# Kernel tuning notes

Hardware: AMD Instinct MI355X
Metric: run time of the kernel (lower is better)

The kernel has to match this reference:

```python
import jax, jax.numpy as jnp
import numpy as np

NUM_HEADS = 16
H_SELF = 10  # hardcoded h in forward: first 10 heads self-attend, rest cross-attend
DIM = 1024
HEAD_DIM = DIM // NUM_HEADS
SCALE = HEAD_DIM ** -0.5


def _qkv(x, Wqkv):
    # x: [B, N, C] -> q, k, v each [B, H, N, hd]
    B, N, C = x.shape
    qkv = (x @ Wqkv).reshape(B, N, 3, NUM_HEADS, C // NUM_HEADS).transpose(2, 0, 3, 1, 4)
    return qkv[0], qkv[1], qkv[2]


def _attn(q, k, v):
    # q,k,v: [B, h, N, d]
    scores = jnp.einsum('bhqd,bhkd->bhqk', q, k) * SCALE
    probs = jax.nn.softmax(scores, axis=-1)  # attn_drop_ratio = 0.0
    return jnp.einsum('bhqk,bhkd->bhqd', probs, v)


def _proj(xa, xb, Wproj, bproj):
    # xa: [B, 10, N, d], xb: [B, 6, N, d] -> [B, N, C]
    B = xa.shape[0]
    N = xa.shape[2]
    x = jnp.concatenate([xa, xb], axis=1).transpose(0, 2, 1, 3).reshape(B, N, DIM)
    return x @ Wproj + bproj  # proj_drop_ratio = 0.0


def setup_inputs() -> dict:
    key = jax.random.key(0)
    k0, k1, k2, k3 = jax.random.split(key, 4)
    B, N, C = 16, 577, DIM
    x1 = jax.random.normal(k0, (B, N, C), dtype=jnp.float32)
    x2 = jax.random.normal(k1, (B, N, C), dtype=jnp.float32)
    # nn.Linear(dim, dim*3, bias=False): store as [C, 3C] so y = x @ W
    Wqkv = jax.random.normal(k2, (C, 3 * C), dtype=jnp.float32) * 0.02
    # nn.Linear(dim, dim) has bias by default
    Wproj = jax.random.normal(k3, (C, C), dtype=jnp.float32) * 0.02
    bproj = jnp.zeros((C,), dtype=jnp.float32)
    return {"x1": x1, "x2": x2, "Wqkv": Wqkv, "Wproj": Wproj, "bproj": bproj}


def reference(x1, x2, Wqkv, Wproj, bproj):
    q1, k1, v1 = _qkv(x1, Wqkv)
    q2, k2, v2 = _qkv(x2, Wqkv)
    h = H_SELF
    x11 = _attn(q1[:, :h], k1[:, :h], v1[:, :h])  # self-attn branch of x1
    x12 = _attn(q1[:, h:], k2[:, h:], v2[:, h:])  # cross: q from x1, kv from x2
    x22 = _attn(q2[:, :h], k2[:, :h], v2[:, :h])  # self-attn branch of x2
    x21 = _attn(q2[:, h:], k1[:, h:], v1[:, h:])  # cross: q from x2, kv from x1
    out1 = _proj(x11, x12, Wproj, bproj)
    out2 = _proj(x22, x21, Wproj, bproj)
    return (out1, out2)
```

## Files before the change

### kernel.cpp

```cpp
#include <hip/hip_runtime.h>
#include <hip/hip_bf16.h>
#include <stdint.h>
#include <math.h>

typedef __attribute__((ext_vector_type(8))) short bf16x8;
typedef __attribute__((ext_vector_type(4))) float f32x4;
typedef __attribute__((ext_vector_type(8))) unsigned short ushort8;
typedef __attribute__((ext_vector_type(4))) unsigned int uint4v;
typedef __attribute__((ext_vector_type(2))) unsigned int uint2v;

#define NTOK   9232
#define MROWS  18464
#define MPAD   18688
#define NPADV  640
#define QSCALE 0.18033688011112042f

__device__ __forceinline__ uint16_t f2b(float f) {
  uint32_t u = __builtin_bit_cast(uint32_t, f);
  u += 0x7fffu + ((u >> 16) & 1u);
  return (uint16_t)(u >> 16);
}

__device__ __forceinline__ uint32_t packbf(float lo, float hi) {
  return (uint32_t)f2b(lo) | ((uint32_t)f2b(hi) << 16);
}

__device__ __forceinline__ f32x4 mfma16(bf16x8 a, bf16x8 b, f32x4 c) {
  return __builtin_amdgcn_mfma_f32_16x16x32_bf16(a, b, c, 0, 0, 0);
}

__device__ __forceinline__ void gl_lds16(const void* g, void* l) {
  __builtin_amdgcn_global_load_lds(
      (const __attribute__((address_space(1))) uint32_t*)g,
      (__attribute__((address_space(3))) uint32_t*)l, 16, 0, 0);
}

__global__ void convert_x_kernel(const float* __restrict__ x1,
                                 const float* __restrict__ x2,
                                 uint16_t* __restrict__ Xb) {
  const size_t stride = (size_t)gridDim.x * blockDim.x;
  const size_t total8 = (size_t)MPAD * 1024 / 8;
  for (size_t i = (size_t)blockIdx.x * blockDim.x + threadIdx.x; i < total8; i += stride) {
    const size_t e = i * 8;
    const size_t row = e >> 10;
    ushort8 ov;
    if (row < (size_t)MROWS) {
      const float* src = (row < (size_t)NTOK) ? (x1 + e) : (x2 + (e - (size_t)NTOK * 1024));
      float4 a = *(const float4*)(src);
      float4 b = *(const float4*)(src + 4);
      ov[0] = f2b(a.x); ov[1] = f2b(a.y); ov[2] = f2b(a.z); ov[3] = f2b(a.w);
      ov[4] = f2b(b.x); ov[5] = f2b(b.y); ov[6] = f2b(b.z); ov[7] = f2b(b.w);
    } else {
      ov = (ushort8)0;
    }
    *(ushort8*)(Xb + e) = ov;
  }
}

__global__ void transw_kernel(const float* __restrict__ in, uint16_t* __restrict__ out,
                              int R, int Cc) {
  __shared__ float t[32][33];
  const int r0 = blockIdx.x * 32, c0 = blockIdx.y * 32;
  const int tr = threadIdx.x >> 5, tc = threadIdx.x & 31;
#pragma unroll
  for (int i = 0; i < 4; ++i)
    t[tr + i * 8][tc] = in[(size_t)(r0 + tr + i * 8) * Cc + c0 + tc];
  __syncthreads();
#pragma unroll
  for (int i = 0; i < 4; ++i) {
    const int orow = c0 + tr + i * 8;
    out[(size_t)orow * R + r0 + tc] = f2b(t[tc][tr + i * 8]);
  }
}

__global__ void zero_vpad_kernel(uint16_t* __restrict__ Vtb) {
  const int idx = blockIdx.x * 256 + threadIdx.x;
  for (int i = idx; i < 32768 * 8; i += 256 * 256) {
    const int p = i >> 3;
    const int ch = i & 7;
    *(ushort8*)(Vtb + (size_t)p * NPADV + 576 + ch * 8) = (ushort8)0;
  }
}

#define G256_SETUP                                                             \
  const int srow = tt >> 2;                                        \
  const int schunk = tt & 3;                         \
  const int swc = schunk ^ ((srow >> 1) & 3);                                  \
  const int crs = (c >> 1) & 3;                                                \
  char* aL = (char*)As3;                                                       \
  char* bL = (char*)Bs3;                                                       \
  auto SA = [&](int buf, int t) {                                              \
    _Pragma("unroll")                                                          \
    for (int i = 0; i < 2; ++i) {                                              \
      const int row = i * 128 + srow;                                          \
      gl_lds16(aG + (size_t)row * 2048 + t * 64 + (swc << 4),                  \
               aL + buf * 16384 + row * 64 + (schunk << 4));                   \
    }                                                                          \
  };                                                                           \
  auto SB = [&](int buf, int t) {                                              \
    _Pragma("unroll")                                                          \
    for (int i = 0; i < 2; ++i) {                                              \
      const int row = i * 128 + srow;                                          \
      gl_lds16(bG + (size_t)row * 2048 + t * 64 + (swc << 4),                  \
               bL + buf * 16384 + row * 64 + (schunk << 4));                   \
    }                                                                          \
  };                                                                           \
  auto LDA = [&](int buf, int mi) -> bf16x8 {                                  \
    const int r = wm * 128 + mi * 16 + c;                                      \
    return *(const bf16x8*)(aL + buf * 16384 + r * 64 + ((g ^ crs) << 4));     \
  };                                                                           \
  auto LDB = [&](int buf, int ni) -> bf16x8 {                                  \
    const int r = wn * 64 + ni * 16 + c;                                       \
    return *(const bf16x8*)(bL + buf * 16384 + r * 64 + ((g ^ crs) << 4));     \
  };

#define G256_MFMA_BLOCK(BR)                                                    \
  {                                                                            \
    bf16x8 b0 = LDB(BR, 0), b1 = LDB(BR, 1);                                   \
    bf16x8 b2 = LDB(BR, 2), b3 = LDB(BR, 3);                                   \
    __builtin_amdgcn_s_setprio(1);                                             \
    _Pragma("unroll")                                                          \
    for (int mi = 0; mi < 8; ++mi) {                                           \
      const bf16x8 a0 = LDA(BR, mi);                                           \
      acc[mi][0] = mfma16(a0, b0, acc[mi][0]);                                 \
      acc[mi][1] = mfma16(a0, b1, acc[mi][1]);                                 \
      acc[mi][2] = mfma16(a0, b2, acc[mi][2]);                                 \
      acc[mi][3] = mfma16(a0, b3, acc[mi][3]);                                 \
    }                                                                          \
    __builtin_amdgcn_s_setprio(0);                                             \
  }

#define G256_ITER_S(T, BR, BS)                                                 \
  {                                                                            \
    asm volatile("s_waitcnt vmcnt(4)" ::: "memory");                           \
    __builtin_amdgcn_s_barrier();                                              \
    __builtin_amdgcn_sched_barrier(0);                                         \
    SA(BS, (T) + 2); SB(BS, (T) + 2);                                          \
    G256_MFMA_BLOCK(BR)                                                        \
  }

#define G256_ITER_N(BR, VM)                                                    \
  {                                                                            \
    asm volatile("s_waitcnt vmcnt(" #VM ")" ::: "memory");                     \
    __builtin_amdgcn_s_barrier();                                              \
    __builtin_amdgcn_sched_barrier(0);                                         \
    G256_MFMA_BLOCK(BR)                                                        \
  }

#define G256_KLOOP                                                             \
  G256_SETUP                                                                   \
  SA(0, 0); SB(0, 0); SA(1, 1); SB(1, 1);                                      \
  for (int j = 0; j < 10; ++j) {                                               \
    const int t3 = j * 3;                                                      \
    G256_ITER_S(t3, 0, 2)                                                      \
    G256_ITER_S(t3 + 1, 1, 0)                                                  \
    G256_ITER_S(t3 + 2, 2, 1)                                                  \
  }                                                                            \
  G256_ITER_N(0, 4)                                                            \
  G256_ITER_N(1, 0)

__global__ __launch_bounds__(512, 1) void gemm_qkv_kernel(
    const uint16_t* __restrict__ A, const uint16_t* __restrict__ Bt,
    uint16_t* __restrict__ Qb, uint16_t* __restrict__ Kb, uint16_t* __restrict__ Vtb) {
  __shared__ __align__(128) char smem[98304];
  uint16_t* As3 = (uint16_t*)smem;
  uint16_t* Bs3 = (uint16_t*)(smem + 49152);
  const int tt = threadIdx.x;
  const int w = tt >> 6, l = tt & 63;
  const int c = l & 15, g = l >> 4;
  const int wm = w >> 2, wn = w & 3;
  const int orig = blockIdx.x;
  const int xcd = orig & 7, sub8 = orig >> 3;
  const int work = (xcd < 4 ? xcd * 110 : 440 + (xcd - 4) * 109) + sub8;
  int bm, bn;
  {
    const int stripe = work / 36;
    if (stripe >= 24) { bm = 72; bn = work - 864; }
    else {
      const int r2 = work % 36;
      const int bg = r2 / 12, r3 = r2 % 12;
      bm = stripe * 3 + r3 % 3;
      bn = bg * 4 + r3 / 3;
    }
  }
  f32x4 acc[8][4] = {};
  const char* aG = (const char*)(A + (size_t)bm * 256 * 1024);
  const char* bG = (const char*)(Bt + (size_t)bn * 256 * 1024);

  G256_KLOOP

  const int sArea = bn >> 2;
  __syncthreads();
  if (sArea <= 1) {
    uint16_t* outb = (sArea == 0) ? Qb : Kb;
    const float scale = (sArea == 0) ? QSCALE : 1.0f;
#pragma unroll
    for (int half = 0; half < 2; ++half) {
      if (wm == half) {
        char* wbase = smem + (g * 4) * 544 + (wn * 64 + c) * 2;
#pragma unroll
        for (int mi = 0; mi < 8; ++mi)
#pragma unroll
          for (int r = 0; r < 4; ++r)
#pragma unroll
            for (int ni = 0; ni < 4; ++ni)
              *(uint16_t*)(wbase + mi * 8704 + r * 544 + ni * 32) =
                  f2b(acc[mi][ni][r] * scale);
      }
      __syncthreads();
      {
        const int row = tt >> 2, hp = tt & 3;
        const int R = bm * 256 + half * 128 + row;
        if (R < MROWS) {
          const int src = (R >= NTOK) ? 1 : 0;
          const int rr = R - src * NTOK;
          const int bb = rr / 577;
          const int nn = rr - bb * 577;
          const size_t base0 =
              ((((size_t)src * 16 + bb) * 16 + (bn & 3) * 4) * 577 + nn) * 64;
          const char* rbase = smem + row * 544;
#pragma unroll
          for (int j = 0; j < 8; ++j) {
            const int ch = hp + j * 4;
            const int hh2 = ch >> 3;
            const int dd = (ch & 7) * 8;
            const uint4v v = *(const uint4v*)(rbase + ch * 16);
            *(uint4v*)(outb + base0 + (size_t)hh2 * 577 * 64 + dd) = v;
          }
        }
      }
      __syncthreads();
    }
  } else {
#pragma unroll
    for (int half = 0; half < 2; ++half) {
      if (wm == half) {
        char* wbase = smem + (wn * 64 + c) * 272 + g * 8;
#pragma unroll
        for (int mi = 0; mi < 8; ++mi)
#pragma unroll
          for (int ni = 0; ni < 4; ++ni) {
            const uint2v pw = {packbf(acc[mi][ni][0], acc[mi][ni][1]),
                               packbf(acc[mi][ni][2], acc[mi][ni][3])};
            *(uint2v*)(wbase + ni * 4352 + mi * 32) = pw;
          }
      }
      __syncthreads();
      {
        const int col = tt >> 1, chh = tt & 1;
        const int C = bn * 256 + col;
        const int hh2 = (C >> 6) & 15;
        const int dd = C & 63;
        const char* rbase = smem + col * 272 + chh * 128;
#pragma unroll
        for (int j = 0; j < 8; ++j) {
          const int R0 = bm * 256 + half * 128 + chh * 64 + j * 8;
          if (R0 >= MROWS) continue;
          const int src0 = (R0 >= NTOK) ? 1 : 0;
          const int rr0 = R0 - src0 * NTOK;
          const int bb0 = rr0 / 577;
          const int nn0 = rr0 - bb0 * 577;
          const uint4v v = *(const uint4v*)(rbase + j * 16);
          const uint16_t* pv = (const uint16_t*)&v;
          const bool fast = (R0 + 7 < MROWS) && (nn0 + 8 <= 577) &&
                            (((R0 + 7) >= NTOK ? 1 : 0) == src0);
          if (fast) {
            uint16_t* dst =
                Vtb + ((((size_t)src0 * 16 + bb0) * 16 + hh2) * 64 + dd) * NPADV + nn0;
#pragma unroll
            for (int e = 0; e < 8; ++e) dst[e] = pv[e];
          } else {
#pragma unroll
            for (int e = 0; e < 8; ++e) {
              const int R = R0 + e;
              if (R >= MROWS) break;
              const int s = (R >= NTOK) ? 1 : 0;
              const int rr = R - s * NTOK;
              const int b2 = rr / 577;
              const int n2 = rr - b2 * 577;
              Vtb[((((size_t)s * 16 + b2) * 16 + hh2) * 64 + dd) * NPADV + n2] = pv[e];
            }
          }
        }
      }
      __syncthreads();
    }
  }
}

#define GEMM_TRI_SETUP                                                         \
  const int srow4 = tt >> 2;                                        \
  const int schunk = tt & 3;                         \
  const int swc = schunk ^ ((srow4 >> 1) & 3);                                 \
  const int crs = (c >> 1) & 3;                                                \
  char* aL = (char*)As3;                                                       \
  char* bL = (char*)Bs3;                                                       \
  auto SA = [&](int buf, int t) {                                              \
    _Pragma("unroll")                                                          \
    for (int i = 0; i < 2; ++i) {                                              \
      const int row = i * 64 + srow4;                                          \
      gl_lds16(aG + (size_t)row * 2048 + t * 64 + (swc << 4),                  \
               aL + buf * 8192 + row * 64 + (schunk << 4));                    \
    }                                                                          \
  };                                                                           \
  auto SB = [&](int buf, int t) {                                              \
    _Pragma("unroll")                                                          \
    for (int i = 0; i < 2; ++i) {                                              \
      const int row = i * 64 + srow4;                                          \
      gl_lds16(bG + (size_t)row * 2048 + t * 64 + (swc << 4),                  \
               bL + buf * 8192 + row * 64 + (schunk << 4));                    \
    }                                                                          \
  };                                                                           \
  auto LDA = [&](int buf, int mi) -> bf16x8 {                                  \
    const int r = wm * 64 + mi * 16 + c;                                       \
    return *(const bf16x8*)(aL + buf * 8192 + r * 64 + ((g ^ crs) << 4));      \
  };                                                                           \
  auto LDB = [&](int buf, int ni) -> bf16x8 {                                  \
    const int r = wn * 64 + ni * 16 + c;                                       \
    return *(const bf16x8*)(bL + buf * 8192 + r * 64 + ((g ^ crs) << 4));      \
  };

#define G_MFMA_BLOCK(BR)                                                       \
  {                                                                            \
    bf16x8 b0 = LDB(BR, 0), b1 = LDB(BR, 1);                                   \
    bf16x8 b2 = LDB(BR, 2), b3 = LDB(BR, 3);                                   \
    __builtin_amdgcn_s_setprio(1);                                             \
    _Pragma("unroll")                                                          \
    for (int mi = 0; mi < 4; ++mi) {                                           \
      const bf16x8 a0 = LDA(BR, mi);                                           \
      acc[mi][0] = mfma16(a0, b0, acc[mi][0]);                                 \
      acc[mi][1] = mfma16(a0, b1, acc[mi][1]);                                 \
      acc[mi][2] = mfma16(a0, b2, acc[mi][2]);                                 \
      acc[mi][3] = mfma16(a0, b3, acc[mi][3]);                                 \
    }                                                                          \
    __builtin_amdgcn_s_setprio(0);                                             \
  }

#define G_ITER_S(T, BR, BS)                                                    \
  {                                                                            \
    asm volatile("s_waitcnt vmcnt(4)" ::: "memory");                           \
    __builtin_amdgcn_s_barrier();                                              \
    __builtin_amdgcn_sched_barrier(0);                                         \
    SA(BS, (T) + 2); SB(BS, (T) + 2);                                          \
    G_MFMA_BLOCK(BR)                                                           \
  }

#define G_ITER_N(BR, VM)                                                       \
  {                                                                            \
    asm volatile("s_waitcnt vmcnt(" #VM ")" ::: "memory");                     \
    __builtin_amdgcn_s_barrier();                                              \
    __builtin_amdgcn_sched_barrier(0);                                         \
    G_MFMA_BLOCK(BR)                                                           \
  }

#define GEMM_TRI_KLOOP                                                         \
  GEMM_TRI_SETUP                                                               \
  SA(0, 0); SB(0, 0); SA(1, 1); SB(1, 1);                                      \
  for (int j = 0; j < 10; ++j) {                                               \
    const int t3 = j * 3;                                                      \
    G_ITER_S(t3, 0, 2)                                                         \
    G_ITER_S(t3 + 1, 1, 0)                                                     \
    G_ITER_S(t3 + 2, 2, 1)                                                     \
  }                                                                            \
  G_ITER_N(0, 4)                                                               \
  G_ITER_N(1, 0)

#define KVB 64
#define ATT_NT 10
__global__ __launch_bounds__(256, 2) void attn_kernel(
    const uint16_t* __restrict__ Qb, const uint16_t* __restrict__ Kb,
    const uint16_t* __restrict__ Vtb, uint16_t* __restrict__ O) {
  __shared__ __align__(128) char smem[73728];
  const int tid = threadIdx.x;
  const int w = tid >> 6, l = tid & 63;
  const int c = l & 15, g = l >> 4;
  const int bid = blockIdx.x;
  const int qc = bid & 1;
  const int p = bid >> 1;
  const int h = p & 15, b = (p >> 4) & 15, o = p >> 8;
  const int kvsrc = (h < 10) ? o : (1 - o);
  const uint16_t* qp = Qb + (((size_t)o * 16 + b) * 16 + h) * 577 * 64;
  const uint16_t* kp = Kb + (((size_t)kvsrc * 16 + b) * 16 + h) * 577 * 64;
  const uint16_t* vp = Vtb + (((size_t)kvsrc * 16 + b) * 16 + h) * 64 * NPADV;

  const int qbase = qc * 320 + w * 80;

  const int sub = l >> 3;
  const int colEl = (((l & 7) ^ sub) << 3);
  char* KsA = smem;
  char* VsA = smem + 16384;
  char* Pb  = smem + 32768 + w * 10240;
  const int rs = (c & 7) << 4;

  bf16x8 Qf[5][2];
#pragma unroll
  for (int qt = 0; qt < 5; ++qt) {
    const int qrow = min(qbase + qt * 16 + c, 576);
    const uint16_t* qr = qp + (size_t)qrow * 64 + g * 8;
    Qf[qt][0] = *(const bf16x8*)(qr);
    Qf[qt][1] = *(const bf16x8*)(qr + 32);
  }

  f32x4 acc[4][5] = {};
  float m_run[5] = {-3.0e38f, -3.0e38f, -3.0e38f, -3.0e38f, -3.0e38f};
  float l_run[5] = {0.f, 0.f, 0.f, 0.f, 0.f};

  auto STAGE = [&](int buf, int kv0) {
#pragma unroll
    for (int i = 0; i < 2; ++i) {
      const int j = w * 2 + i;
      const int row = j * 8 + sub;
      const int gk = min(kv0 + row, 576);
      gl_lds16(kp + (size_t)gk * 64 + colEl, KsA + buf * 8192 + j * 1024 + l * 16);
      gl_lds16(vp + (size_t)row * NPADV + kv0 + colEl, VsA + buf * 8192 + j * 1024 + l * 16);
    }
  };

  STAGE(0, 0);
  __syncthreads();

  for (int t = 0; t < ATT_NT; ++t) {
    if (t < ATT_NT - 1) STAGE((t + 1) & 1, (t + 1) * KVB);
    {
      const char* Kt = KsA + (t & 1) * 8192;
      const char* Vt = VsA + (t & 1) * 8192;
      bf16x8 Kf[4][2];
#pragma unroll
      for (int kt = 0; kt < 4; ++kt) {
        const char* kr = Kt + (kt * 16 + c) * 128;
        Kf[kt][0] = *(const bf16x8*)(kr + ((g * 16) ^ rs));
        Kf[kt][1] = *(const bf16x8*)(kr + ((64 + g * 16) ^ rs));
      }
      float alpha_[5];
#pragma unroll
      for (int qt = 0; qt < 5; ++qt) {
        f32x4 s[4];
#pragma unroll
        for (int kt = 0; kt < 4; ++kt) {
          f32x4 z = {0.f, 0.f, 0.f, 0.f};
          z = mfma16(Kf[kt][0], Qf[qt][0], z);
          z = mfma16(Kf[kt][1], Qf[qt][1], z);
          s[kt] = z;
        }
        if (t == ATT_NT - 1) {
#pragma unroll
          for (int kt = 0; kt < 4; ++kt)
#pragma unroll
            for (int r = 0; r < 4; ++r) {
              if (kt == 0 && r == 0) { if (g > 0) s[kt][r] = -3.0e38f; }
              else s[kt][r] = -3.0e38f;
            }
        }
        float mt = s[0][0];
#pragma unroll
        for (int kt = 0; kt < 4; ++kt)
#pragma unroll
          for (int r = 0; r < 4; ++r) mt = fmaxf(mt, s[kt][r]);
        mt = fmaxf(mt, __shfl_xor(mt, 16));
        mt = fmaxf(mt, __shfl_xor(mt, 32));
        const float mnew = fmaxf(m_run[qt], mt);
        const float al = exp2f(m_run[qt] - mnew);
        m_run[qt] = mnew;
        alpha_[qt] = al;
        float lt = 0.f;
#pragma unroll
        for (int kt = 0; kt < 4; ++kt)
#pragma unroll
          for (int r = 0; r < 4; ++r) {
            const float pv = exp2f(s[kt][r] - mnew);
            s[kt][r] = pv;
            lt += pv;
          }
        lt += __shfl_xor(lt, 16);
        lt += __shfl_xor(lt, 32);
        l_run[qt] = l_run[qt] * al + lt;
        const int rowOff = (qt * 16 + c) * 128;
#pragma unroll
        for (int kt = 0; kt < 4; ++kt) {
          const uint2v pw = {packbf(s[kt][0], s[kt][1]), packbf(s[kt][2], s[kt][3])};
          *(uint2v*)(Pb + rowOff + ((kt * 32 + g * 8) ^ rs)) = pw;
        }
      }
#pragma unroll
      for (int dt = 0; dt < 4; ++dt)
#pragma unroll
        for (int qt = 0; qt < 5; ++qt)
#pragma unroll
          for (int r = 0; r < 4; ++r) acc[dt][qt][r] *= alpha_[qt];
      bf16x8 pf[5][2];
#pragma unroll
      for (int qt = 0; qt < 5; ++qt) {
        const char* pr = Pb + (qt * 16 + c) * 128;
        pf[qt][0] = *(const bf16x8*)(pr + ((g * 16) ^ rs));
        pf[qt][1] = *(const bf16x8*)(pr + ((64 + g * 16) ^ rs));
      }
#pragma unroll
      for (int dt = 0; dt < 4; ++dt) {
        const char* vr = Vt + (dt * 16 + c) * 128;
        const bf16x8 v0 = *(const bf16x8*)(vr + ((g * 16) ^ rs));
        const bf16x8 v1 = *(const bf16x8*)(vr + ((64 + g * 16) ^ rs));
#pragma unroll
        for (int qt = 0; qt < 5; ++qt) {
          acc[dt][qt] = mfma16(v0, pf[qt][0], acc[dt][qt]);
          acc[dt][qt] = mfma16(v1, pf[qt][1], acc[dt][qt]);
        }
      }
    }
    __syncthreads();
  }

  {
#pragma unroll
    for (int qt = 0; qt < 5; ++qt) {
      const float inv = 1.0f / l_run[qt];
      const int rowOff = (qt * 16 + c) * 128;
#pragma unroll
      for (int dt = 0; dt < 4; ++dt) {
        const uint2v pw = {packbf(acc[dt][qt][0] * inv, acc[dt][qt][1] * inv),
                           packbf(acc[dt][qt][2] * inv, acc[dt][qt][3] * inv)};
        *(uint2v*)(Pb + rowOff + ((dt * 32 + g * 8) ^ rs)) = pw;
      }
    }
    const size_t obase = ((size_t)o * NTOK + (size_t)b * 577) * 1024 + h * 64;
#pragma unroll
    for (int pass = 0; pass < 10; ++pass) {
      const int row = pass * 8 + (l >> 3);
      const int tok = qbase + row;
      const uint4v vv = *(const uint4v*)(Pb + row * 128 + (((l & 7) * 16) ^ ((row & 7) << 4)));
      if (tok <= 576)
        *(uint4v*)(O + obase + (size_t)tok * 1024 + (l & 7) * 8) = vv;
    }
  }
}

__global__ __launch_bounds__(256, 3) void gemm_proj_kernel(
    const uint16_t* __restrict__ A, const uint16_t* __restrict__ Bt,
    const float* __restrict__ bias, float* __restrict__ out) {
  __shared__ uint16_t As3[3][4096];
  __shared__ uint16_t Bs3[3][4096];
  const int tt = threadIdx.x;
  const int w = tt >> 6, l = tt & 63;
  const int c = l & 15, g = l >> 4;
  const int wgid = blockIdx.x;
  const int work = (wgid & 7) * 145 + (wgid >> 3);
  int bm, bn;
  {
    const int stripe = work / 48;
    if (stripe >= 24) { bm = 144; bn = work - 24 * 48; }
    else { const int r3 = work % 48; bm = stripe * 6 + r3 % 6; bn = r3 / 6; }
  }
  const int wm = w >> 1, wn = w & 1;
  f32x4 acc[4][4] = {};
  const char* aG = (const char*)(A + (size_t)bm * 128 * 1024);
  const char* bG = (const char*)(Bt + (size_t)bn * 128 * 1024);

  GEMM_TRI_KLOOP

#pragma unroll
  for (int mi = 0; mi < 4; ++mi) {
#pragma unroll
    for (int r = 0; r < 4; ++r) {
      const int R = bm * 128 + wm * 64 + mi * 16 + g * 4 + r;
      if (R >= MROWS) continue;
#pragma unroll
      for (int ni = 0; ni < 4; ++ni) {
        const int C = bn * 128 + wn * 64 + ni * 16 + c;
        out[(size_t)R * 1024 + C] = acc[mi][ni][r] + bias[C];
      }
    }
  }
}

extern "C" void kernel_launch(void* const* d_in, const int* in_sizes, int n_in,
                              void* d_out, int out_size, void* d_ws, size_t ws_size,
                              hipStream_t stream) {
  (void)in_sizes; (void)n_in; (void)out_size; (void)ws_size;
  const float* x1    = (const float*)d_in[0];
  const float* x2    = (const float*)d_in[1];
  const float* Wqkv  = (const float*)d_in[2];
  const float* Wproj = (const float*)d_in[3];
  const float* bproj = (const float*)d_in[4];
  float* out = (float*)d_out;

  char* ws = (char*)d_ws;
  size_t off = 0;
  auto alloc = [&](size_t bytes) -> char* {
    char* p = ws + off;
    off += (bytes + 255) & ~(size_t)255;
    return p;
  };
  uint16_t* Xb     = (uint16_t*)alloc((size_t)MPAD * 1024 * 2);
  uint16_t* Wqkvt  = (uint16_t*)alloc((size_t)3072 * 1024 * 2);
  uint16_t* Wprojt = (uint16_t*)alloc((size_t)1024 * 1024 * 2);
  uint16_t* Qb     = (uint16_t*)alloc((size_t)512 * 577 * 64 * 2);
  uint16_t* Kb     = (uint16_t*)alloc((size_t)512 * 577 * 64 * 2);
  uint16_t* Vtb    = (uint16_t*)alloc((size_t)512 * 64 * NPADV * 2);

  zero_vpad_kernel<<<256, 256, 0, stream>>>(Vtb);
  convert_x_kernel<<<2048, 256, 0, stream>>>(x1, x2, Xb);
  transw_kernel<<<dim3(32, 96), 256, 0, stream>>>(Wqkv, Wqkvt, 1024, 3072);
  transw_kernel<<<dim3(32, 32), 256, 0, stream>>>(Wproj, Wprojt, 1024, 1024);
  gemm_qkv_kernel<<<876, 512, 0, stream>>>(Xb, Wqkvt, Qb, Kb, Vtb);
  attn_kernel<<<1024, 256, 0, stream>>>(Qb, Kb, Vtb, Xb );
  gemm_proj_kernel<<<1160, 256, 0, stream>>>(Xb, Wprojt, bproj, out);
}
```

Before: 363.3 us.

## Shrink QKV GEMM LDS to double buffering to raise blocks per CU

The QKV projection GEMM moves from a three-stage LDS ring with partial vmcnt waits to a two-stage double buffer that waits on vmcnt(0) every k-step. Shared memory drops from 96KB to 64KB. The epilogue staging is split into quarter and half tiles so it fits the smaller buffer. Launch bounds are raised to request more resident blocks per CU, trading load-latency hiding inside a block for more concurrency across blocks. The tighter register budget may force the 128-float accumulator to spill, and the full drain each step adds stalls.

```diff
diff --git a/kernel.cpp b/kernel.cpp
--- a/kernel.cpp
+++ b/kernel.cpp
@@ -130,41 +130,29 @@
     __builtin_amdgcn_s_setprio(0);                                             \
   }
 
-#define G256_ITER_S(T, BR, BS)                                                 \
+#define G256R2_ITER(T, BR)                                                     \
   {                                                                            \
-    asm volatile("s_waitcnt vmcnt(4)" ::: "memory");                           \
+    asm volatile("s_waitcnt vmcnt(0)" ::: "memory");                           \
     __builtin_amdgcn_s_barrier();                                              \
     __builtin_amdgcn_sched_barrier(0);                                         \
-    SA(BS, (T) + 2); SB(BS, (T) + 2);                                          \
-    G256_MFMA_BLOCK(BR)                                                        \
-  }
-
-#define G256_ITER_N(BR, VM)                                                    \
-  {                                                                            \
-    asm volatile("s_waitcnt vmcnt(" #VM ")" ::: "memory");                     \
-    __builtin_amdgcn_s_barrier();                                              \
-    __builtin_amdgcn_sched_barrier(0);                                         \
+    if ((T) < 31) { SA((BR) ^ 1, (T) + 1); SB((BR) ^ 1, (T) + 1); }            \
     G256_MFMA_BLOCK(BR)                                                        \
   }
 
 #define G256_KLOOP                                                             \
   G256_SETUP                                                                   \
-  SA(0, 0); SB(0, 0); SA(1, 1); SB(1, 1);                                      \
-  for (int j = 0; j < 10; ++j) {                                               \
-    const int t3 = j * 3;                                                      \
-    G256_ITER_S(t3, 0, 2)                                                      \
-    G256_ITER_S(t3 + 1, 1, 0)                                                  \
-    G256_ITER_S(t3 + 2, 2, 1)                                                  \
-  }                                                                            \
-  G256_ITER_N(0, 4)                                                            \
-  G256_ITER_N(1, 0)
-
-__global__ __launch_bounds__(512, 1) void gemm_qkv_kernel(
+  SA(0, 0); SB(0, 0);                                                          \
+  for (int j2 = 0; j2 < 16; ++j2) {                                            \
+    G256R2_ITER(2 * j2, 0)                                                     \
+    G256R2_ITER(2 * j2 + 1, 1)                                                 \
+  }
+
+__global__ __launch_bounds__(512, 4) void gemm_qkv_kernel(
     const uint16_t* __restrict__ A, const uint16_t* __restrict__ Bt,
     uint16_t* __restrict__ Qb, uint16_t* __restrict__ Kb, uint16_t* __restrict__ Vtb) {
-  __shared__ __align__(128) char smem[98304];
+  __shared__ __align__(128) char smem[65536];
   uint16_t* As3 = (uint16_t*)smem;
-  uint16_t* Bs3 = (uint16_t*)(smem + 49152);
+  uint16_t* Bs3 = (uint16_t*)(smem + 32768);
   const int tt = threadIdx.x;
   const int w = tt >> 6, l = tt & 63;
   const int c = l & 15, g = l >> 4;
@@ -195,22 +183,24 @@
     uint16_t* outb = (sArea == 0) ? Qb : Kb;
     const float scale = (sArea == 0) ? QSCALE : 1.0f;
 #pragma unroll
-    for (int half = 0; half < 2; ++half) {
-      if (wm == half) {
+    for (int q = 0; q < 4; ++q) {
+      if (wm == (q >> 1)) {
         char* wbase = smem + (g * 4) * 544 + (wn * 64 + c) * 2;
 #pragma unroll
-        for (int mi = 0; mi < 8; ++mi)
+        for (int mi2 = 0; mi2 < 4; ++mi2) {
+          const int mi = (q & 1) * 4 + mi2;
 #pragma unroll
           for (int r = 0; r < 4; ++r)
 #pragma unroll
             for (int ni = 0; ni < 4; ++ni)
-              *(uint16_t*)(wbase + mi * 8704 + r * 544 + ni * 32) =
+              *(uint16_t*)(wbase + mi2 * 8704 + r * 544 + ni * 32) =
                   f2b(acc[mi][ni][r] * scale);
+        }
       }
       __syncthreads();
       {
-        const int row = tt >> 2, hp = tt & 3;
-        const int R = bm * 256 + half * 128 + row;
+        const int row = tt >> 3, hp = tt & 7;
+        const int R = bm * 256 + q * 64 + row;
         if (R < MROWS) {
           const int src = (R >= NTOK) ? 1 : 0;
           const int rr = R - src * NTOK;
@@ -220,8 +210,8 @@
               ((((size_t)src * 16 + bb) * 16 + (bn & 3) * 4) * 577 + nn) * 64;
           const char* rbase = smem + row * 544;
 #pragma unroll
-          for (int j = 0; j < 8; ++j) {
-            const int ch = hp + j * 4;
+          for (int j = 0; j < 4; ++j) {
+            const int ch = hp + j * 8;
             const int hh2 = ch >> 3;
             const int dd = (ch & 7) * 8;
             const uint4v v = *(const uint4v*)(rbase + ch * 16);
@@ -234,56 +224,59 @@
   } else {
 #pragma unroll
     for (int half = 0; half < 2; ++half) {
-      if (wm == half) {
-        char* wbase = smem + (wn * 64 + c) * 272 + g * 8;
-#pragma unroll
-        for (int mi = 0; mi < 8; ++mi)
-#pragma unroll
-          for (int ni = 0; ni < 4; ++ni) {
-            const uint2v pw = {packbf(acc[mi][ni][0], acc[mi][ni][1]),
-                               packbf(acc[mi][ni][2], acc[mi][ni][3])};
-            *(uint2v*)(wbase + ni * 4352 + mi * 32) = pw;
-          }
-      }
-      __syncthreads();
-      {
-        const int col = tt >> 1, chh = tt & 1;
-        const int C = bn * 256 + col;
-        const int hh2 = (C >> 6) & 15;
-        const int dd = C & 63;
-        const char* rbase = smem + col * 272 + chh * 128;
-#pragma unroll
-        for (int j = 0; j < 8; ++j) {
-          const int R0 = bm * 256 + half * 128 + chh * 64 + j * 8;
-          if (R0 >= MROWS) continue;
-          const int src0 = (R0 >= NTOK) ? 1 : 0;
-          const int rr0 = R0 - src0 * NTOK;
-          const int bb0 = rr0 / 577;
-          const int nn0 = rr0 - bb0 * 577;
-          const uint4v v = *(const uint4v*)(rbase + j * 16);
-          const uint16_t* pv = (const uint16_t*)&v;
-          const bool fast = (R0 + 7 < MROWS) && (nn0 + 8 <= 577) &&
-                            (((R0 + 7) >= NTOK ? 1 : 0) == src0);
-          if (fast) {
-            uint16_t* dst =
-                Vtb + ((((size_t)src0 * 16 + bb0) * 16 + hh2) * 64 + dd) * NPADV + nn0;
-#pragma unroll
-            for (int e = 0; e < 8; ++e) dst[e] = pv[e];
-          } else {
-#pragma unroll
-            for (int e = 0; e < 8; ++e) {
-              const int R = R0 + e;
-              if (R >= MROWS) break;
-              const int s = (R >= NTOK) ? 1 : 0;
-              const int rr = R - s * NTOK;
-              const int b2 = rr / 577;
-              const int n2 = rr - b2 * 577;
-              Vtb[((((size_t)s * 16 + b2) * 16 + hh2) * 64 + dd) * NPADV + n2] = pv[e];
+#pragma unroll
+      for (int hv = 0; hv < 2; ++hv) {
+        if (wm == half && (wn >> 1) == hv) {
+          char* wbase = smem + ((wn & 1) * 64 + c) * 272 + g * 8;
+#pragma unroll
+          for (int mi = 0; mi < 8; ++mi)
+#pragma unroll
+            for (int ni = 0; ni < 4; ++ni) {
+              const uint2v pw = {packbf(acc[mi][ni][0], acc[mi][ni][1]),
+                                 packbf(acc[mi][ni][2], acc[mi][ni][3])};
+              *(uint2v*)(wbase + ni * 4352 + mi * 32) = pw;
+            }
+        }
+        __syncthreads();
+        {
+          const int col = tt >> 2, s = tt & 3;
+          const int C = bn * 256 + hv * 128 + col;
+          const int hh2 = (C >> 6) & 15;
+          const int dd = C & 63;
+          const char* rbase = smem + col * 272 + s * 64;
+#pragma unroll
+          for (int j = 0; j < 4; ++j) {
+            const int R0 = bm * 256 + half * 128 + s * 32 + j * 8;
+            if (R0 >= MROWS) continue;
+            const int src0 = (R0 >= NTOK) ? 1 : 0;
+            const int rr0 = R0 - src0 * NTOK;
+            const int bb0 = rr0 / 577;
+            const int nn0 = rr0 - bb0 * 577;
+            const uint4v v = *(const uint4v*)(rbase + j * 16);
+            const uint16_t* pv = (const uint16_t*)&v;
+            const bool fast = (R0 + 7 < MROWS) && (nn0 + 8 <= 577) &&
+                              (((R0 + 7) >= NTOK ? 1 : 0) == src0);
+            if (fast) {
+              uint16_t* dst =
+                  Vtb + ((((size_t)src0 * 16 + bb0) * 16 + hh2) * 64 + dd) * NPADV + nn0;
+#pragma unroll
+              for (int e = 0; e < 8; ++e) dst[e] = pv[e];
+            } else {
+#pragma unroll
+              for (int e = 0; e < 8; ++e) {
+                const int R = R0 + e;
+                if (R >= MROWS) break;
+                const int sx = (R >= NTOK) ? 1 : 0;
+                const int rr = R - sx * NTOK;
+                const int b2 = rr / 577;
+                const int n2 = rr - b2 * 577;
+                Vtb[((((size_t)sx * 16 + b2) * 16 + hh2) * 64 + dd) * NPADV + n2] = pv[e];
+              }
             }
           }
         }
-      }
-      __syncthreads();
+        __syncthreads();
+      }
     }
   }
 }
```

Result: slower. 1.001 ms (+175.5%).
